# Optimization experiments

Hardware: AMD Instinct MI355X
Metric: run time of the kernel (lower is better)

Reference implementation:

```python
import jax, jax.numpy as jnp
import numpy as np

B, M, D, E, N, K = 4, 4096, 768, 1536, 16, 3


def _layernorm(x, g, b, eps=1e-5):
    mu = x.mean(-1, keepdims=True)
    var = ((x - mu) ** 2).mean(-1, keepdims=True)
    return (x - mu) * jax.lax.rsqrt(var + eps) * g + b


def _conv1d(x, w, b):
    # x: (B, E, M), w: (E_out, E_in, K), 'same' padding like Conv1d(padding=k//2)
    p = w.shape[-1] // 2
    y = jax.lax.conv_general_dilated(x, w, window_strides=(1,), padding=[(p, p)],
                                     dimension_numbers=('NCH', 'OIH', 'NCH'))
    return y + b[None, :, None]


def _scan_ssm(xp, A_base, WB, bB, WC, bC, WD, bD, dbias, reverse):
    # xp: (B, M, E); faithful to source: h = (Delta*A_base)*h + (Delta*B)*x, y = sum_n h*C
    if reverse:
        xp = xp[:, ::-1]
    Bp = jnp.einsum('bme,ne->bmn', xp, WB) + bB          # (B, M, N)
    Cp = jnp.einsum('bme,ne->bmn', xp, WC) + bC          # (B, M, N)
    Delta = jax.nn.softplus(jnp.einsum('bme,fe->bmf', xp, WD) + bD + dbias)  # (B, M, E)
    h0 = jnp.zeros((xp.shape[0], A_base.shape[0], A_base.shape[1]), xp.dtype)

    def step(h, inp):
        x_i, d_i, b_i, c_i = inp  # (B,E), (B,E), (B,N), (B,N)
        h = (d_i[..., None] * A_base) * h + (d_i * x_i)[..., None] * b_i[:, None, :]
        return h, jnp.einsum('ben,bn->be', h, c_i)

    xs = tuple(jnp.swapaxes(a, 0, 1) for a in (xp, Delta, Bp, Cp))  # time-major
    _, ys = jax.lax.scan(step, h0, xs)
    y = jnp.swapaxes(ys, 0, 1)  # (B, M, E)
    return y[:, ::-1] if reverse else y


def setup_inputs() -> dict:
    key = jax.random.key(0)
    ks = jax.random.split(key, 16)
    rn = lambda k, shape, s=0.02: jax.random.normal(k, shape, jnp.float32) * s
    return {
        't': jax.random.normal(ks[0], (B, M, D), jnp.float32),
        'ln_g': jnp.ones((D,), jnp.float32), 'ln_b': jnp.zeros((D,), jnp.float32),
        'Wx': rn(ks[1], (E, D)), 'bx': jnp.zeros((E,), jnp.float32),
        'Wz': rn(ks[2], (E, D)), 'bz': jnp.zeros((E,), jnp.float32),
        'Wcf': rn(ks[3], (E, E, K)), 'bcf': jnp.zeros((E,), jnp.float32),
        'Wcb': rn(ks[4], (E, E, K)), 'bcb': jnp.zeros((E,), jnp.float32),
        'WBf': rn(ks[5], (N, E)), 'bBf': jnp.zeros((N,), jnp.float32),
        'WCf': rn(ks[6], (N, E)), 'bCf': jnp.zeros((N,), jnp.float32),
        'WDf': rn(ks[7], (E, E)), 'bDf': jnp.zeros((E,), jnp.float32),
        'WBb': rn(ks[8], (N, E)), 'bBb': jnp.zeros((N,), jnp.float32),
        'WCb': rn(ks[9], (N, E)), 'bCb': jnp.zeros((N,), jnp.float32),
        'WDb': rn(ks[10], (E, E)), 'bDb': jnp.zeros((E,), jnp.float32),
        'Abf': rn(ks[11], (E, N), 0.01), 'Abb': rn(ks[12], (E, N), 0.01),
        'dbf': jnp.zeros((E,), jnp.float32), 'dbb': jnp.zeros((E,), jnp.float32),
        'WT': rn(ks[13], (D, E)), 'bT': jnp.zeros((D,), jnp.float32),
    }


def reference(t, ln_g, ln_b, Wx, bx, Wz, bz, Wcf, bcf, Wcb, bcb,
              WBf, bBf, WCf, bCf, WDf, bDf, WBb, bBb, WCb, bCb, WDb, bDb,
              Abf, Abb, dbf, dbb, WT, bT):
    residual = t
    xn = _layernorm(t, ln_g, ln_b)
    x_proj = xn @ Wx.T + bx        # (B, M, E)
    z = xn @ Wz.T + bz             # (B, M, E)
    xc = jnp.swapaxes(x_proj, 1, 2)
    xp_f = jax.nn.silu(jnp.swapaxes(_conv1d(xc, Wcf, bcf), 1, 2))
    xp_b = jax.nn.silu(jnp.swapaxes(_conv1d(xc, Wcb, bcb), 1, 2))
    y_f = _scan_ssm(xp_f, Abf, WBf, bBf, WCf, bCf, WDf, bDf, dbf, False)
    y_b = _scan_ssm(xp_b, Abb, WBb, bBb, WCb, bCb, WDb, bDb, dbb, True)
    y = (y_f + y_b) * jax.nn.silu(z)
    return y @ WT.T + bT + residual
```

## Files before the change

### kernel.cpp

```cpp
#include <hip/hip_runtime.h>

#define BB 4
#define MM 4096
#define DD 768
#define EE 1536
#define NX 1664
#define BMROWS 16384
#define SCAN_C 128
#define SCAN_W 12

typedef __attribute__((ext_vector_type(8))) short short8;
typedef __attribute__((ext_vector_type(4))) float f32x4;

#define GLD16(src, dst)                                                   \
  __builtin_amdgcn_global_load_lds(                                       \
      (const __attribute__((address_space(1))) void*)(src),               \
      (__attribute__((address_space(3))) void*)(dst), 16, 0, 0)

__device__ __forceinline__ float bf2f(unsigned short u) {
  union { unsigned int i; float f; } v; v.i = ((unsigned int)u) << 16; return v.f;
}
__device__ __forceinline__ unsigned short f2bf(float f) {
  if (f != f) f = 0.f;
  union { float f; unsigned int i; } v; v.f = f;
  unsigned int x = v.i;
  return (unsigned short)((x + 0x7FFFu + ((x >> 16) & 1u)) >> 16);
}
__device__ __forceinline__ float silu_f(float v) { return v / (1.f + __expf(-v)); }
__device__ __forceinline__ float softplus_f(float v) {
  return (v > 15.f) ? v : log1pf(__expf(v));
}

__global__ __launch_bounds__(256) void detect_kernel(const float* __restrict__ t,
                                                     int* __restrict__ flag) {
  __shared__ int cnt[256];
  int c = 0;
  for (int j = 0; j < 64; j++) {
    float v = t[j * 256 + threadIdx.x];
    float a = fabsf(v);
    bool sane = (v == 0.0f) || (a > 9.09e-13f && a < 1.1e12f);
    c += sane ? 1 : 0;
  }
  cnt[threadIdx.x] = c;
  __syncthreads();
  if (threadIdx.x == 0) {
    int s = 0;
    for (int i = 0; i < 256; i++) s += cnt[i];
    flag[0] = (s > 14746) ? 1 : 0;
  }
}

struct NormArgs {
  const void* src[26];
  unsigned short* dst[26];
  int n[26];
  int cb[26];
};

__global__ __launch_bounds__(256) void normalize_all_kernel(NormArgs args,
                                                            const int* __restrict__ flag) {
  const int f = flag[0];
  const int blk = blockIdx.x;
  int t = 0;
#pragma unroll 1
  for (int i = 1; i < 26; ++i)
    if (blk >= args.cb[i]) t = i;
  const void* src = args.src[t];
  unsigned short* dst = args.dst[t];
  const int n = args.n[t];
  const int base = (blk - args.cb[t]) * 1024 + threadIdx.x * 4;
#pragma unroll
  for (int j = 0; j < 4; ++j) {
    const int k = base + j;
    if (k < n)
      dst[k] = f ? f2bf(((const float*)src)[k]) : ((const unsigned short*)src)[k];
  }
}

__global__ __launch_bounds__(256) void zero_kernel(unsigned short* __restrict__ p, int n) {
  const int i = blockIdx.x * 256 + threadIdx.x;
  if (i < n) p[i] = 0;
}

__global__ __launch_bounds__(256) void ln_kernel(
    const void* __restrict__ t, const unsigned short* __restrict__ gam,
    const unsigned short* __restrict__ bet, unsigned short* __restrict__ xn,
    const int* __restrict__ flag) {
  const int row = blockIdx.x, tid = threadIdx.x;
  const int f = flag[0];
  float x0, x1, x2;
  if (f) {
    const float* tr = (const float*)t + (size_t)row * DD;
    x0 = tr[tid]; x1 = tr[tid + 256]; x2 = tr[tid + 512];
  } else {
    const unsigned short* tr = (const unsigned short*)t + (size_t)row * DD;
    x0 = bf2f(tr[tid]); x1 = bf2f(tr[tid + 256]); x2 = bf2f(tr[tid + 512]);
  }
  float s = x0 + x1 + x2;
  float s2 = x0 * x0 + x1 * x1 + x2 * x2;
#pragma unroll
  for (int o = 32; o > 0; o >>= 1) {
    s += __shfl_xor(s, o, 64);
    s2 += __shfl_xor(s2, o, 64);
  }
  __shared__ float rs[4], rs2[4];
  if ((tid & 63) == 0) { rs[tid >> 6] = s; rs2[tid >> 6] = s2; }
  __syncthreads();
  float S = rs[0] + rs[1] + rs[2] + rs[3];
  float S2 = rs2[0] + rs2[1] + rs2[2] + rs2[3];
  float mu = S * (1.f / 768.f);
  float var = fmaxf(S2 * (1.f / 768.f) - mu * mu, 0.f);
  float rstd = rsqrtf(var + 1e-5f);
  unsigned short* xo = xn + (size_t)row * DD;
  xo[tid]       = f2bf((x0 - mu) * rstd * bf2f(gam[tid])       + bf2f(bet[tid]));
  xo[tid + 256] = f2bf((x1 - mu) * rstd * bf2f(gam[tid + 256]) + bf2f(bet[tid + 256]));
  xo[tid + 512] = f2bf((x2 - mu) * rstd * bf2f(gam[tid + 512]) + bf2f(bet[tid + 512]));
}

__global__ __launch_bounds__(256) void repack_kernel(
    const void* __restrict__ W, unsigned short* __restrict__ Wk,
    const int* __restrict__ flag) {
  size_t idx = (size_t)blockIdx.x * 256 + threadIdx.x;
  const size_t tot = (size_t)3 * EE * EE;
  if (idx < tot) {
    int i = (int)(idx % EE);
    int rest = (int)(idx / EE);
    int o = rest % EE;
    int k = rest / EE;
    size_t s = ((size_t)o * EE + i) * 3 + k;
    Wk[idx] = flag[0] ? f2bf(((const float*)W)[s]) : ((const unsigned short*)W)[s];
  }
}

template <int EPI, int TAPS>
__global__ __launch_bounds__(256, 4) void gemm_bt(
    const unsigned short* __restrict__ A, const unsigned short* __restrict__ Bw,
    const unsigned short* __restrict__ bias1, const unsigned short* __restrict__ bias2,
    const unsigned short* __restrict__ resid16, const float* __restrict__ residf,
    unsigned short* __restrict__ Cb16, float* __restrict__ Cf32,
    int Mrows, int N, int K,
    const unsigned short* __restrict__ zpad, const int* __restrict__ oflag) {
  constexpr int LSA = (TAPS == 3) ? 130 * 32 : 128 * 64;
  constexpr int LSB = (TAPS == 3) ? 3 * 128 * 32 : 128 * 64;
  __shared__ __align__(16) unsigned short lsA[LSA];
  __shared__ __align__(16) unsigned short lsB[LSB];
  const int tid = threadIdx.x;
  const int tm = blockIdx.x * 128;
  const int tn = blockIdx.y * 128;
  const int lane = tid & 63;
  const int wave = tid >> 6;
  const int wm = (wave >> 1) * 64, wn = (wave & 1) * 64;
  const int lm = lane & 15, q = lane >> 4;

  f32x4 acc[4][4];
#pragma unroll
  for (int i = 0; i < 4; i++)
#pragma unroll
    for (int j = 0; j < 4; j++) acc[i][j] = (f32x4){0.f, 0.f, 0.f, 0.f};

  const short8 zero8 = (short8){0, 0, 0, 0, 0, 0, 0, 0};

  if (TAPS == 3) {
    int aoffc[4], boffc[4];
#pragma unroll
    for (int f = 0; f < 4; f++) {
      aoffc[f] = (wm + f * 16 + lm) * 32 + q * 8;
      boffc[f] = (wn + f * 16 + lm) * 32 + q * 8;
    }
    const int lo = (tm / MM) * MM;
    const int hi = lo + MM;
    for (int k0 = 0; k0 < K; k0 += 32) {
#pragma unroll
      for (int i = 0; i < 2; i++) {
        const int idx = i * 256 + tid;
        GLD16(A + (size_t)(tm + (idx >> 2)) * K + k0 + (idx & 3) * 8,
              lsA + 32 + idx * 8);
      }
      if (tid < 8) {
        const int hs = tid >> 2;
        const int ch = tid & 3;
        const int grow = hs ? (tm + 128) : (tm - 1);
        const bool ok = (grow >= lo) && (grow < hi);
        const short8 v = ok ? *(const short8*)(A + (size_t)grow * K + k0 + ch * 8)
                            : zero8;
        *(short8*)(lsA + (hs ? 129 : 0) * 32 + ch * 8) = v;
      }
#pragma unroll
      for (int t = 0; t < 3; ++t) {
        const unsigned short* Bt = Bw + (size_t)t * N * K;
#pragma unroll
        for (int i = 0; i < 2; i++) {
          const int idx = i * 256 + tid;
          GLD16(Bt + (size_t)(tn + (idx >> 2)) * K + k0 + (idx & 3) * 8,
                lsB + t * 4096 + idx * 8);
        }
      }
      __syncthreads();
#pragma unroll
      for (int tap = 0; tap < 3; ++tap) {
        short8 af[4], bfr[4];
#pragma unroll
        for (int f = 0; f < 4; f++)
          af[f] = *(const short8*)(lsA + aoffc[f] + tap * 32);
#pragma unroll
        for (int f = 0; f < 4; f++)
          bfr[f] = *(const short8*)(lsB + tap * 4096 + boffc[f]);
#pragma unroll
        for (int i = 0; i < 4; i++)
#pragma unroll
          for (int j = 0; j < 4; j++)
            acc[i][j] = __builtin_amdgcn_mfma_f32_16x16x32_bf16(af[i], bfr[j], acc[i][j], 0, 0, 0);
      }
      __syncthreads();
    }
  } else {
    const int sr = tid >> 3;
    const int gs = tid & 7;
    int aoff[2][4], boff[2][4];
#pragma unroll
    for (int s = 0; s < 2; s++)
#pragma unroll
      for (int f = 0; f < 4; f++) {
        aoff[s][f] = (wm + f * 16 + lm) * 64 + (s * 4 + q) * 8;
        boff[s][f] = (wn + f * 16 + lm) * 64 + (s * 4 + q) * 8;
      }
    for (int k0 = 0; k0 < K; k0 += 64) {
      const int kc = k0 + gs * 8;
#pragma unroll
      for (int i = 0; i < 4; i++) {
        const int r = i * 32 + sr;
        GLD16(A + (size_t)(tm + r) * K + kc, lsA + r * 64 + gs * 8);
        GLD16(Bw + (size_t)(tn + r) * K + kc, lsB + r * 64 + gs * 8);
      }
      __syncthreads();
#pragma unroll
      for (int s = 0; s < 2; s++) {
        short8 af[4], bfr[4];
#pragma unroll
        for (int f = 0; f < 4; f++) af[f] = *(const short8*)(lsA + aoff[s][f]);
#pragma unroll
        for (int f = 0; f < 4; f++) bfr[f] = *(const short8*)(lsB + boff[s][f]);
#pragma unroll
        for (int i = 0; i < 4; i++)
#pragma unroll
          for (int j = 0; j < 4; j++)
            acc[i][j] = __builtin_amdgcn_mfma_f32_16x16x32_bf16(af[i], bfr[j], acc[i][j], 0, 0, 0);
      }
      __syncthreads();
    }
  }

#pragma unroll
  for (int i = 0; i < 4; i++) {
#pragma unroll
    for (int j = 0; j < 4; j++) {
      int col = tn + wn + j * 16 + lm;
      if (EPI == 4) {
        if (col < EE) {
          float badd = bf2f(bias1[col]) + bf2f(bias2[col]);
#pragma unroll
          for (int r = 0; r < 4; r++) {
            int row = tm + wm + i * 16 + q * 4 + r;
            float v = softplus_f(acc[i][j][r] + badd);
            Cb16[(size_t)row * EE + col] = f2bf(v);
          }
        } else if (col < EE + 32) {
          float badd = bf2f(resid16[col - EE]);
#pragma unroll
          for (int r = 0; r < 4; r++) {
            int row = tm + wm + i * 16 + q * 4 + r;
            Cf32[(size_t)row * 32 + (col - EE)] = acc[i][j][r] + badd;
          }
        }
        continue;
      }
      float badd = bf2f(bias1[col]);
      if (EPI == 2) badd += bf2f(bias2[col]);
#pragma unroll
      for (int r = 0; r < 4; r++) {
        int row = tm + wm + i * 16 + q * 4 + r;
        float v = acc[i][j][r] + badd;
        if (EPI == 1) v = silu_f(v);
        if (EPI == 2) v = softplus_f(v);
        const size_t oi = (size_t)row * N + col;
        if (EPI == 3) {
          const int f = oflag[0];
          v += f ? residf[oi] : bf2f(resid16[oi]);
          if (f) Cf32[oi] = (v != v) ? 0.f : v;
          else   Cb16[oi] = f2bf(v);
        } else {
          Cb16[oi] = f2bf(v);
        }
      }
    }
  }
}

__global__ __launch_bounds__(256) void scan_kernel(
    const unsigned short* __restrict__ Delta, const unsigned short* __restrict__ xp,
    const float* __restrict__ BC,
    const unsigned short* __restrict__ Aen, const unsigned short* __restrict__ yprev,
    const unsigned short* sz, unsigned short* yout, int dir) {
  const size_t bo = (size_t)blockIdx.z * MM * EE;
  const size_t bo32 = (size_t)blockIdx.z * MM * 32;
  Delta += bo; xp += bo; yout += bo;
  BC += bo32;
  if (yprev) yprev += bo;
  if (sz) sz += bo;

  const int e = blockIdx.x * 256 + threadIdx.x;
  const int chunk = blockIdx.y;
  const int L = MM / SCAN_C;
  const int p0 = chunk * L;
  const int pw = (chunk == 0) ? 0 : p0 - SCAN_W;
  const int p1 = p0 + L;

  float a[16], h[16];
#pragma unroll
  for (int n = 0; n < 16; n++) {
    a[n] = bf2f(Aen[(size_t)e * 16 + n]);
    h[n] = 0.f;
  }

  int m = dir ? (MM - 1 - pw) : pw;
  float d = bf2f(Delta[(size_t)m * EE + e]);
  float x = bf2f(xp[(size_t)m * EE + e]);
  float bv[16];
  {
    const float4* bp = (const float4*)(BC + (size_t)m * 32);
    *(float4*)&bv[0] = bp[0]; *(float4*)&bv[4] = bp[1];
    *(float4*)&bv[8] = bp[2]; *(float4*)&bv[12] = bp[3];
  }

  for (int p = pw; p < p1; ++p) {
    float dn = 0.f, xnv = 0.f, bn[16];
    if (p + 1 < p1) {
      const int mn = dir ? (MM - 1 - (p + 1)) : (p + 1);
      dn = bf2f(Delta[(size_t)mn * EE + e]);
      xnv = bf2f(xp[(size_t)mn * EE + e]);
      const float4* bp = (const float4*)(BC + (size_t)mn * 32);
      *(float4*)&bn[0] = bp[0]; *(float4*)&bn[4] = bp[1];
      *(float4*)&bn[8] = bp[2]; *(float4*)&bn[12] = bp[3];
    }

    const float dx = d * x;
#pragma unroll
    for (int n = 0; n < 16; n++) h[n] = d * a[n] * h[n] + dx * bv[n];

    if (p >= p0) {
      const int mc = dir ? (MM - 1 - p) : p;
      const float4* cp = (const float4*)(BC + (size_t)mc * 32 + 16);
      float cv[16];
      *(float4*)&cv[0] = cp[0]; *(float4*)&cv[4] = cp[1];
      *(float4*)&cv[8] = cp[2]; *(float4*)&cv[12] = cp[3];
      float y0 = 0.f, y1 = 0.f, y2 = 0.f, y3 = 0.f;
#pragma unroll
      for (int n = 0; n < 16; n += 4) {
        y0 += h[n] * cv[n]; y1 += h[n + 1] * cv[n + 1];
        y2 += h[n + 2] * cv[n + 2]; y3 += h[n + 3] * cv[n + 3];
      }
      const float y = (y0 + y1) + (y2 + y3);
      const size_t idx = (size_t)mc * EE + e;
      if (dir == 0) {
        yout[idx] = f2bf(y);
      } else {
        const float g = (bf2f(yprev[idx]) + y) * bf2f(sz[idx]);
        yout[idx] = f2bf(g);
      }
    }

    d = dn; x = xnv;
#pragma unroll
    for (int n = 0; n < 16; n++) bv[n] = bn[n];
  }
}

extern "C" void kernel_launch(void* const* d_in, const int* in_sizes, int n_in,
                              void* d_out, int out_size, void* d_ws, size_t ws_size,
                              hipStream_t stream) {
  (void)n_in; (void)out_size;

  size_t cur = 0;
  auto alloc_us = [&](size_t n) {
    unsigned short* p = (unsigned short*)d_ws + cur;
    cur += (n + 7) & ~(size_t)7;
    return p;
  };
  int* dflag = (int*)alloc_us(16);
  unsigned short* xn   = alloc_us((size_t)BMROWS * DD);
  unsigned short* nlng = alloc_us(DD);
  unsigned short* nlnb = alloc_us(DD);
  unsigned short* nWx  = alloc_us((size_t)EE * DD);
  unsigned short* nbx  = alloc_us(EE);
  unsigned short* nWz  = alloc_us((size_t)EE * DD);
  unsigned short* nbz  = alloc_us(EE);
  unsigned short* nbcf = alloc_us(EE);
  unsigned short* nbcb = alloc_us(EE);
  unsigned short* nWDXf = alloc_us((size_t)NX * EE);
  unsigned short* nWDXb = alloc_us((size_t)NX * EE);
  unsigned short* nbDf = alloc_us(EE);
  unsigned short* nbDb = alloc_us(EE);
  unsigned short* nbBCf = alloc_us(32);
  unsigned short* nbBCb = alloc_us(32);
  unsigned short* nAbf = alloc_us((size_t)EE * 16);
  unsigned short* nAbb = alloc_us((size_t)EE * 16);
  unsigned short* ndbf = alloc_us(EE);
  unsigned short* ndbb = alloc_us(EE);
  unsigned short* nWT  = alloc_us((size_t)DD * EE);
  unsigned short* nbT  = alloc_us(DD);
  const size_t WK = (size_t)3 * EE * EE;
  unsigned short* wkF  = alloc_us(WK);
  unsigned short* wkB  = alloc_us(WK);
  unsigned short* zpad = alloc_us(1536);

  const size_t avail = (ws_size / 2 > cur) ? (ws_size / 2 - cur) : 0;
  int G = 1;
  {
    auto need = [&](int g) {
      return (size_t)4 * ((size_t)g * MM * EE) + 2 * ((size_t)g * MM * 64) + 1024;
    };
    if (need(4) <= avail) G = 4;
    else if (need(2) <= avail) G = 2;
  }
  const size_t R = (size_t)G * MM;
  unsigned short* U1 = alloc_us(R * EE);
  unsigned short* U2 = alloc_us(R * EE);
  unsigned short* U3 = alloc_us(R * EE);
  unsigned short* U4 = alloc_us(R * EE);
  float* BCF = (float*)alloc_us(R * 64);
  float* BCB = (float*)alloc_us(R * 64);

  detect_kernel<<<1, 256, 0, stream>>>((const float*)d_in[0], dflag);
  {
    NormArgs na;
    const int idxs[26] = {1, 2, 3, 4, 5, 6, 8, 10, 11, 12, 13, 14, 15, 16,
                          17, 18, 19, 20, 21, 22, 23, 24, 25, 26, 27, 28};
    unsigned short* dsts[26] = {
        nlng, nlnb, nWx, nbx, nWz, nbz, nbcf, nbcb,
        nWDXf + (size_t)1536 * EE,
        nbBCf,
        nWDXf + (size_t)1552 * EE,
        nbBCf + 16,
        nWDXf,
        nbDf,
        nWDXb + (size_t)1536 * EE,
        nbBCb,
        nWDXb + (size_t)1552 * EE,
        nbBCb + 16,
        nWDXb,
        nbDb,
        nAbf, nAbb, ndbf, ndbb, nWT, nbT};
    int cb = 0;
    for (int i = 0; i < 26; ++i) {
      na.src[i] = d_in[idxs[i]];
      na.dst[i] = dsts[i];
      na.n[i] = in_sizes[idxs[i]];
      na.cb[i] = cb;
      cb += (in_sizes[idxs[i]] + 1023) / 1024;
    }
    normalize_all_kernel<<<cb, 256, 0, stream>>>(na, dflag);
  }
  zero_kernel<<<6, 256, 0, stream>>>(zpad, 1536);
  {
    const int zn = 96 * EE;
    zero_kernel<<<(zn + 255) / 256, 256, 0, stream>>>(nWDXf + (size_t)1568 * EE, zn);
    zero_kernel<<<(zn + 255) / 256, 256, 0, stream>>>(nWDXb + (size_t)1568 * EE, zn);
  }
  const int rp_blocks = (int)((WK + 255) / 256);
  repack_kernel<<<rp_blocks, 256, 0, stream>>>(d_in[7], wkF, dflag);
  repack_kernel<<<rp_blocks, 256, 0, stream>>>(d_in[9], wkB, dflag);

  ln_kernel<<<BMROWS, 256, 0, stream>>>(d_in[0], nlng, nlnb, xn, dflag);

  const int Mr = (int)R;
  const dim3 gE(Mr / 128, EE / 128);
  const dim3 gX(Mr / 128, NX / 128);
  const dim3 gD(Mr / 128, DD / 128);
  const dim3 gScan(EE / 256, SCAN_C, G);
  const int nGroups = BB / G;

  for (int g = 0; g < nGroups; ++g) {
    const unsigned short* xn_g = xn + (size_t)g * R * DD;
    const unsigned short* res16 = (const unsigned short*)d_in[0] + (size_t)g * R * DD;
    const float*          res32 = (const float*)d_in[0] + (size_t)g * R * DD;
    unsigned short* outb_b16 = (unsigned short*)d_out + (size_t)g * R * DD;
    float*          outb_f32 = (float*)d_out + (size_t)g * R * DD;

    gemm_bt<0, 1><<<gE, 256, 0, stream>>>(xn_g, nWx, nbx, nullptr, nullptr, nullptr,
                                          U1, nullptr, Mr, EE, DD, zpad, dflag);
    gemm_bt<1, 3><<<gE, 256, 0, stream>>>(U1, wkF, nbcf, nullptr, nullptr, nullptr,
                                          U2, nullptr, Mr, EE, EE, zpad, dflag);
    gemm_bt<4, 1><<<gX, 256, 0, stream>>>(U2, nWDXf, nbDf, ndbf, nbBCf, nullptr,
                                          U3, BCF, Mr, NX, EE, zpad, dflag);
    scan_kernel<<<gScan, 256, 0, stream>>>(U3, U2, BCF, nAbf,
                                           nullptr, nullptr, U4, 0);
    gemm_bt<1, 3><<<gE, 256, 0, stream>>>(U1, wkB, nbcb, nullptr, nullptr, nullptr,
                                          U3, nullptr, Mr, EE, EE, zpad, dflag);
    gemm_bt<4, 1><<<gX, 256, 0, stream>>>(U3, nWDXb, nbDb, ndbb, nbBCb, nullptr,
                                          U1, BCB, Mr, NX, EE, zpad, dflag);
    gemm_bt<1, 1><<<gE, 256, 0, stream>>>(xn_g, nWz, nbz, nullptr, nullptr, nullptr,
                                          U2, nullptr, Mr, EE, DD, zpad, dflag);
    scan_kernel<<<gScan, 256, 0, stream>>>(U1, U3, BCB, nAbb,
                                           U4, U2, U2, 1);
    gemm_bt<3, 1><<<gD, 256, 0, stream>>>(U2, nWT, nbT, nullptr, res16, res32,
                                          outb_b16, outb_f32, Mr, DD, EE, zpad, dflag);
  }
}
```

Before: 1.647 ms.

## Software-pipeline the conv GEMM with per-tap staging, XOR swizzle and preloaded halo

Rewrites the 3-tap conv GEMM main loop as a software pipeline. Each tap's B slice and the next A tile are issued with global_load_lds while the previous tap computes, and explicit vmcnt waits plus barriers replace the two __syncthreads per iteration. The LDS layout gains an XOR swizzle against bank conflicts, and the full halo rows are loaded once up front instead of every k step. Launch bounds drop to 3 blocks per CU for the larger LDS footprint. This adds hand-tuned waitcnt ordering that is fragile, and the loop is hardcoded for K=1536.

```diff
diff --git a/kernel.cpp b/kernel.cpp
--- a/kernel.cpp
+++ b/kernel.cpp
@@ -16,6 +16,10 @@
   __builtin_amdgcn_global_load_lds(                                       \
       (const __attribute__((address_space(1))) void*)(src),               \
       (__attribute__((address_space(3))) void*)(dst), 16, 0, 0)
+
+#define S_VMCNT(N) asm volatile("s_waitcnt vmcnt(" #N ")" ::: "memory")
+#define S_LGKM0()  asm volatile("s_waitcnt lgkmcnt(0)" ::: "memory")
+#define S_BAR()    __builtin_amdgcn_s_barrier()
 
 __device__ __forceinline__ float bf2f(unsigned short u) {
   union { unsigned int i; float f; } v; v.i = ((unsigned int)u) << 16; return v.f;
@@ -133,17 +137,15 @@
 }
 
 template <int EPI, int TAPS>
-__global__ __launch_bounds__(256, 4) void gemm_bt(
+__global__ __launch_bounds__(256, TAPS == 3 ? 3 : 4) void gemm_bt(
     const unsigned short* __restrict__ A, const unsigned short* __restrict__ Bw,
     const unsigned short* __restrict__ bias1, const unsigned short* __restrict__ bias2,
     const unsigned short* __restrict__ resid16, const float* __restrict__ residf,
     unsigned short* __restrict__ Cb16, float* __restrict__ Cf32,
     int Mrows, int N, int K,
     const unsigned short* __restrict__ zpad, const int* __restrict__ oflag) {
-  constexpr int LSA = (TAPS == 3) ? 130 * 32 : 128 * 64;
-  constexpr int LSB = (TAPS == 3) ? 3 * 128 * 32 : 128 * 64;
-  __shared__ __align__(16) unsigned short lsA[LSA];
-  __shared__ __align__(16) unsigned short lsB[LSB];
+  constexpr int LSTOT = (TAPS == 3) ? 23552 : 2 * 128 * 64;
+  __shared__ __align__(16) unsigned short ls[LSTOT];
   const int tid = threadIdx.x;
   const int tm = blockIdx.x * 128;
   const int tn = blockIdx.y * 128;
@@ -161,59 +163,108 @@
   const short8 zero8 = (short8){0, 0, 0, 0, 0, 0, 0, 0};
 
   if (TAPS == 3) {
-    int aoffc[4], boffc[4];
-#pragma unroll
-    for (int f = 0; f < 4; f++) {
-      aoffc[f] = (wm + f * 16 + lm) * 32 + q * 8;
-      boffc[f] = (wn + f * 16 + lm) * 32 + q * 8;
-    }
+    constexpr int AB0 = 0, AB1 = 4096;
+    constexpr int BB0 = 8192, BB1 = 12288, BB2 = 16384, HB = 20480;
     const int lo = (tm / MM) * MM;
     const int hi = lo + MM;
-    for (int k0 = 0; k0 < K; k0 += 32) {
-#pragma unroll
-      for (int i = 0; i < 2; i++) {
-        const int idx = i * 256 + tid;
-        GLD16(A + (size_t)(tm + (idx >> 2)) * K + k0 + (idx & 3) * 8,
-              lsA + 32 + idx * 8);
-      }
-      if (tid < 8) {
-        const int hs = tid >> 2;
-        const int ch = tid & 3;
-        const int grow = hs ? (tm + 128) : (tm - 1);
-        const bool ok = (grow >= lo) && (grow < hi);
-        const short8 v = ok ? *(const short8*)(A + (size_t)grow * K + k0 + ch * 8)
-                            : zero8;
-        *(short8*)(lsA + (hs ? 129 : 0) * 32 + ch * 8) = v;
-      }
-#pragma unroll
-      for (int t = 0; t < 3; ++t) {
-        const unsigned short* Bt = Bw + (size_t)t * N * K;
-#pragma unroll
-        for (int i = 0; i < 2; i++) {
-          const int idx = i * 256 + tid;
-          GLD16(Bt + (size_t)(tn + (idx >> 2)) * K + k0 + (idx & 3) * 8,
-                lsB + t * 4096 + idx * 8);
+    const size_t NK = (size_t)N * K;
+
+    const int idx0 = tid, idx1 = 256 + tid;
+    const int r0 = idx0 >> 2, c0 = (idx0 & 3) ^ ((idx0 >> 3) & 3);
+    const int r1 = idx1 >> 2, c1 = (idx1 & 3) ^ ((idx1 >> 3) & 3);
+    const unsigned short* pA0 = A + (size_t)(tm + r0) * K + c0 * 8;
+    const unsigned short* pA1 = A + (size_t)(tm + r1) * K + c1 * 8;
+    const unsigned short* pB0 = Bw + (size_t)(tn + r0) * K + c0 * 8;
+    const unsigned short* pB1 = Bw + (size_t)(tn + r1) * K + c1 * 8;
+
+    int boffv[4];
+#pragma unroll
+    for (int f = 0; f < 4; f++) {
+      const int rb = wn + f * 16 + lm;
+      boffv[f] = rb * 32 + (q ^ ((rb >> 1) & 3)) * 8;
+    }
+    int aoffv[3][4], hflag[3][4];
+#pragma unroll
+    for (int tp = 0; tp < 3; tp++)
+#pragma unroll
+      for (int f = 0; f < 4; f++) {
+        const int ra = wm + f * 16 + lm + tp - 1;
+        if (ra < 0)        { hflag[tp][f] = 1; aoffv[tp][f] = HB + q * 8; }
+        else if (ra > 127) { hflag[tp][f] = 1; aoffv[tp][f] = HB + 1536 + q * 8; }
+        else {
+          hflag[tp][f] = 0;
+          aoffv[tp][f] = ra * 32 + (q ^ ((ra >> 1) & 3)) * 8;
         }
       }
-      __syncthreads();
-#pragma unroll
-      for (int tap = 0; tap < 3; ++tap) {
-        short8 af[4], bfr[4];
-#pragma unroll
-        for (int f = 0; f < 4; f++)
-          af[f] = *(const short8*)(lsA + aoffc[f] + tap * 32);
-#pragma unroll
-        for (int f = 0; f < 4; f++)
-          bfr[f] = *(const short8*)(lsB + tap * 4096 + boffc[f]);
-#pragma unroll
-        for (int i = 0; i < 4; i++)
-#pragma unroll
-          for (int j = 0; j < 4; j++)
-            acc[i][j] = __builtin_amdgcn_mfma_f32_16x16x32_bf16(af[i], bfr[j], acc[i][j], 0, 0, 0);
-      }
-      __syncthreads();
-    }
+
+    auto stA = [&](int koff, int aoff) {
+      GLD16(pA0 + koff, ls + aoff + idx0 * 8);
+      GLD16(pA1 + koff, ls + aoff + idx1 * 8);
+    };
+    auto stB = [&](int tap, int koff, int boff) {
+      GLD16(pB0 + (size_t)tap * NK + koff, ls + boff + idx0 * 8);
+      GLD16(pB1 + (size_t)tap * NK + koff, ls + boff + idx1 * 8);
+    };
+    auto comp = [&](int tp, int aoff, int boff, int kh) {
+      short8 af[4], bfr[4];
+#pragma unroll
+      for (int f = 0; f < 4; f++) {
+        const int ad = hflag[tp][f] ? (aoffv[tp][f] + kh) : (aoffv[tp][f] + aoff);
+        af[f] = *(const short8*)(ls + ad);
+      }
+#pragma unroll
+      for (int f = 0; f < 4; f++) bfr[f] = *(const short8*)(ls + boff + boffv[f]);
+#pragma unroll
+      for (int i = 0; i < 4; i++)
+#pragma unroll
+        for (int j = 0; j < 4; j++)
+          acc[i][j] = __builtin_amdgcn_mfma_f32_16x16x32_bf16(af[i], bfr[j], acc[i][j], 0, 0, 0);
+    };
+
+    stA(0, AB0);
+    stB(0, 0, BB0);
+    for (int c = tid; c < 384; c += 256) {
+      const int hs = c / 192;
+      const int kc = (c % 192) * 8;
+      const int grow = hs ? (tm + 128) : (tm - 1);
+      short8 v = zero8;
+      if (grow >= lo && grow < hi) v = *(const short8*)(A + (size_t)grow * K + kc);
+      *(short8*)(ls + HB + hs * 1536 + kc) = v;
+    }
+    __syncthreads();
+
+    int k0 = 0;
+#pragma unroll 1
+    for (int pr = 0; pr < 23; ++pr) {
+      stB(1, k0, BB1);                       S_VMCNT(2); S_BAR();
+      comp(0, AB0, BB0, k0);                 S_LGKM0();
+      stB(2, k0, BB2);                       S_VMCNT(2); S_BAR();
+      comp(1, AB0, BB1, k0);                 S_LGKM0();
+      stA(k0 + 32, AB1); stB(0, k0 + 32, BB0); S_VMCNT(4); S_BAR();
+      comp(2, AB0, BB2, k0);                 S_LGKM0();
+      stB(1, k0 + 32, BB1);                  S_VMCNT(2); S_BAR();
+      comp(0, AB1, BB0, k0 + 32);            S_LGKM0();
+      stB(2, k0 + 32, BB2);                  S_VMCNT(2); S_BAR();
+      comp(1, AB1, BB1, k0 + 32);            S_LGKM0();
+      stA(k0 + 64, AB0); stB(0, k0 + 64, BB0); S_VMCNT(4); S_BAR();
+      comp(2, AB1, BB2, k0 + 32);            S_LGKM0();
+      k0 += 64;
+    }
+    stB(1, k0, BB1);                       S_VMCNT(2); S_BAR();
+    comp(0, AB0, BB0, k0);                 S_LGKM0();
+    stB(2, k0, BB2);                       S_VMCNT(2); S_BAR();
+    comp(1, AB0, BB1, k0);                 S_LGKM0();
+    stA(k0 + 32, AB1); stB(0, k0 + 32, BB0); S_VMCNT(4); S_BAR();
+    comp(2, AB0, BB2, k0);                 S_LGKM0();
+    stB(1, k0 + 32, BB1);                  S_VMCNT(2); S_BAR();
+    comp(0, AB1, BB0, k0 + 32);            S_LGKM0();
+    stB(2, k0 + 32, BB2);                  S_VMCNT(2); S_BAR();
+    comp(1, AB1, BB1, k0 + 32);            S_LGKM0();
+    S_VMCNT(0); S_BAR();
+    comp(2, AB1, BB2, k0 + 32);
   } else {
+    unsigned short* lsA = ls;
+    unsigned short* lsB = ls + 8192;
     const int sr = tid >> 3;
     const int gs = tid & 7;
     int aoff[2][4], boff[2][4];
@@ -294,6 +345,7 @@
       }
     }
   }
+  (void)zpad;
 }
 
 __global__ __launch_bounds__(256) void scan_kernel(
```

Result: slower. 1.765 ms (+7.2%).
